# Kernel tuning notes

Hardware: AMD Instinct MI355X
Metric: run time of the kernel (lower is better)

The kernel has to match this reference:

```python
import jax, jax.numpy as jnp
import numpy as np

N_NODES = 50000
N_EDGES = 800000
H = 128            # node_hidden_size
T = 2              # num_prop_rounds


def setup_inputs() -> dict:
    key = jax.random.key(0)
    ks = jax.random.split(key, 10)
    hv = jax.random.normal(ks[0], (N_NODES, H), dtype=jnp.float32)
    he = jax.random.normal(ks[1], (N_EDGES, 1), dtype=jnp.float32)
    src = jax.random.randint(ks[2], (N_EDGES,), 0, N_NODES, dtype=jnp.int32)
    dst = jax.random.randint(ks[3], (N_EDGES,), 0, N_NODES, dtype=jnp.int32)
    # per-round params, stacked on leading T axis; small scale to avoid gate saturation
    W_msg = jax.random.normal(ks[4], (T, 2 * H, 2 * H + 1), dtype=jnp.float32) * 0.05
    b_msg = jax.random.normal(ks[5], (T, 2 * H), dtype=jnp.float32) * 0.05
    W_ih = jax.random.normal(ks[6], (T, 3 * H, 2 * H), dtype=jnp.float32) * 0.05
    W_hh = jax.random.normal(ks[7], (T, 3 * H, H), dtype=jnp.float32) * 0.05
    b_ih = jax.random.normal(ks[8], (T, 3 * H), dtype=jnp.float32) * 0.05
    b_hh = jax.random.normal(ks[9], (T, 3 * H), dtype=jnp.float32) * 0.05
    return dict(hv=hv, he=he, src=src, dst=dst, W_msg=W_msg, b_msg=b_msg,
                W_ih=W_ih, W_hh=W_hh, b_ih=b_ih, b_hh=b_hh)


def _gru_cell(x, h, W_ih, W_hh, b_ih, b_hh):
    # torch.nn.GRUCell math
    gi = x @ W_ih.T + b_ih          # [N, 3H]
    gh = h @ W_hh.T + b_hh          # [N, 3H]
    i_r, i_z, i_n = jnp.split(gi, 3, axis=1)
    h_r, h_z, h_n = jnp.split(gh, 3, axis=1)
    r = jax.nn.sigmoid(i_r + h_r)
    z = jax.nn.sigmoid(i_z + h_z)
    n = jnp.tanh(i_n + r * h_n)
    return (1.0 - z) * n + z * h


def reference(hv, he, src, dst, W_msg, b_msg, W_ih, W_hh, b_ih, b_hh):
    n_nodes = hv.shape[0]
    for t in range(T):
        # per-edge message input: concat([hv_dst, hv_src, he])  [E, 2H+1]
        msg_in = jnp.concatenate([hv[dst], hv[src], he], axis=1)
        edge_act = msg_in @ W_msg[t].T + b_msg[t]          # [E, 2H]
        # ragged sum-reduce over incoming edges (deg-0 nodes get zeros)
        a = jax.ops.segment_sum(edge_act, dst, num_segments=n_nodes)  # [N, 2H]
        hv = _gru_cell(a, hv, W_ih[t], W_hh[t], b_ih[t], b_hh[t])
    return hv
```

## Files before the change

kernel.cpp:

```cpp
#include <hip/hip_runtime.h>
#include <cstdint>
#include <cstddef>

#define N_NODES 50000
#define N_EDGES 800000
#define HDIM 128
#define TROUNDS 2
#define NTILES 3125
#define PACK_PER_T (416 * 64)
#define MAXDEG 64
#define CSTRIDE 16

typedef __attribute__((ext_vector_type(8))) _Float16 half8v;
typedef __attribute__((ext_vector_type(2))) _Float16 half2v;
typedef __attribute__((ext_vector_type(4))) float f32x4;
typedef unsigned short ushort_t;

#define GLD_LDS(gp, lp)                                                        \
  __builtin_amdgcn_global_load_lds(                                            \
      (__attribute__((address_space(1))) const void*)(gp),                     \
      (__attribute__((address_space(3))) void*)(lp), 16, 0, 0)

static __device__ __forceinline__ float sigmoidf_(float x) {
  return 1.0f / (1.0f + __expf(-x));
}
static __device__ __forceinline__ float tanhf_(float x) {
  float xc = fminf(15.0f, fmaxf(-15.0f, x));
  float a = __expf(2.0f * xc);
  return (a - 1.0f) / (a + 1.0f);
}
static __device__ __forceinline__ float f16bits2f(uint32_t hb) {
  ushort_t u = (ushort_t)hb;
  _Float16 h;
  __builtin_memcpy(&h, &u, 2);
  return (float)h;
}

__global__ void pack_all(const float* __restrict__ Wmsg, const float* __restrict__ Wih,
                         const float* __restrict__ Whh, _Float16* __restrict__ W1p,
                         _Float16* __restrict__ W2p, float* __restrict__ we) {
  int g = blockIdx.x * blockDim.x + threadIdx.x;
  if (g < TROUNDS * 256) {
    int t = g >> 8, j = g & 255;
    we[g] = Wmsg[((size_t)t * 256 + j) * 257 + 256];
  }
  if (g >= TROUNDS * PACK_PER_T) return;
  int t = g / PACK_PER_T;
  int r = g % PACK_PER_T;
  int lane = r & 63;
  int fr = r >> 6;
  const float* srcp;
  _Float16* dstp;
  if (fr < 128) {
    int jt = fr >> 3, kt = fr & 7;
    int j = jt * 16 + (lane & 15);
    int k = kt * 32 + ((lane >> 4) << 3);
    srcp = Wmsg + (size_t)t * 256 * 257 + (size_t)j * 257 + k;
    dstp = W1p + ((size_t)t * 128 + fr) * 512 + lane * 8;
  } else {
    int fr2 = fr - 128;
    int chunk = fr2 / 12, idx = fr2 % 12;
    int jt = chunk / 3, pp = chunk % 3;
    int j = pp * 128 + jt * 16 + (lane & 15);
    int k;
    if (idx < 8) {
      k = idx * 32 + ((lane >> 4) << 3);
      srcp = Wih + (size_t)t * 384 * 256 + (size_t)j * 256 + k;
    } else {
      k = (idx - 8) * 32 + ((lane >> 4) << 3);
      srcp = Whh + (size_t)t * 384 * 128 + (size_t)j * 128 + k;
    }
    dstp = W2p + ((size_t)t * 288 + fr2) * 512 + lane * 8;
  }
  #pragma unroll
  for (int e = 0; e < 8; ++e) dstp[e] = (_Float16)srcp[e];
}

__global__ void cast_hv(const float* __restrict__ hv, _Float16* __restrict__ hvh) {
  int i = blockIdx.x * blockDim.x + threadIdx.x;
  if (i >= N_NODES * HDIM / 4) return;
  float4 v = reinterpret_cast<const float4*>(hv)[i];
  half2v o0, o1;
  o0[0] = (_Float16)v.x; o0[1] = (_Float16)v.y;
  o1[0] = (_Float16)v.z; o1[1] = (_Float16)v.w;
  reinterpret_cast<half2v*>(hvh)[i * 2] = o0;
  reinterpret_cast<half2v*>(hvh)[i * 2 + 1] = o1;
}

__global__ void fill_pad(const int* __restrict__ src, const int* __restrict__ dst,
                         const float* __restrict__ he, int* __restrict__ cnt,
                         uint32_t* __restrict__ csr) {
  int e = blockIdx.x * blockDim.x + threadIdx.x;
  if (e >= N_EDGES) return;
  int d = dst[e];
  int slot = atomicAdd(&cnt[(size_t)d * CSTRIDE], 1);
  if (slot < MAXDEG) {
    _Float16 hh = (_Float16)he[e];
    ushort_t hb;
    __builtin_memcpy(&hb, &hh, 2);
    uint32_t en = ((uint32_t)hb << 16) | (uint32_t)src[e];
    csr[(size_t)d * MAXDEG + slot] = en;
  }
}

__global__ void gather_h(const _Float16* __restrict__ hvh, const int* __restrict__ cnt,
                         const uint32_t* __restrict__ csr, _Float16* __restrict__ S_h,
                         float* __restrict__ hsum, float* __restrict__ deg_f, int n) {
  int wid = (int)((blockIdx.x * blockDim.x + threadIdx.x) >> 6);
  int lane = threadIdx.x & 63;
  if (wid >= n) return;
  int deg = min(cnt[(size_t)wid * CSTRIDE], MAXDEG);
  uint32_t ent = (lane < deg) ? csr[(size_t)wid * MAXDEG + lane] : 0u;
  float a0 = 0.f, a1 = 0.f, hs = 0.f;
  int k = 0;
  for (; k + 7 < deg; k += 8) {
    uint32_t ee[8];
    #pragma unroll
    for (int q = 0; q < 8; ++q) ee[q] = __shfl(ent, k + q);
    half2v vv[8];
    #pragma unroll
    for (int q = 0; q < 8; ++q)
      vv[q] = *reinterpret_cast<const half2v*>(hvh + (size_t)(ee[q] & 0xffffu) * HDIM + lane * 2);
    #pragma unroll
    for (int q = 0; q < 8; ++q) {
      a0 += (float)vv[q][0];
      a1 += (float)vv[q][1];
      hs += f16bits2f(ee[q] >> 16);
    }
  }
  for (; k < deg; ++k) {
    uint32_t e0 = __shfl(ent, k);
    half2v v0 = *reinterpret_cast<const half2v*>(hvh + (size_t)(e0 & 0xffffu) * HDIM + lane * 2);
    a0 += (float)v0[0];
    a1 += (float)v0[1];
    hs += f16bits2f(e0 >> 16);
  }
  half2v o;
  o[0] = (_Float16)a0;
  o[1] = (_Float16)a1;
  *reinterpret_cast<half2v*>(S_h + (size_t)wid * HDIM + lane * 2) = o;
  if (lane == 0) hsum[wid] = hs;
  if (lane == 1) deg_f[wid] = (float)deg;
}

__global__ __launch_bounds__(256, 4) void u1_kernel(
    const float* __restrict__ hv, const _Float16* __restrict__ S_h,
    const float* __restrict__ deg_f, const float* __restrict__ hsum,
    const _Float16* __restrict__ W1p, const float* __restrict__ we,
    const float* __restrict__ bmsg, _Float16* __restrict__ a_out) {
  __shared__ _Float16 buf[2][8 * 512];
  const int tid = threadIdx.x;
  const int wv = tid >> 6, lane = tid & 63;
  const int tile = blockIdx.x * 4 + wv;
  const bool act = (tile < NTILES);
  const int rowA = tile * 16 + (lane & 15);
  const int koff = (lane >> 4) * 8;
  const int m0 = (lane >> 4) * 4;

  {
    const _Float16* g = W1p + (size_t)(wv * 2) * 512 + lane * 8;
    #pragma unroll
    for (int i = 0; i < 2; ++i) GLD_LDS(g + i * 512, &buf[0][(wv * 2 + i) * 512]);
  }

  half8v x[8];
  float degs[4], hss[4];
  if (act) {
    float deg = deg_f[rowA];
    const float* hrow = hv + (size_t)rowA * HDIM;
    #pragma unroll
    for (int kt = 0; kt < 4; ++kt) {
      const float* sp = hrow + kt * 32 + koff;
      #pragma unroll
      for (int e = 0; e < 8; ++e) x[kt][e] = (_Float16)(sp[e] * deg);
    }
    const _Float16* srow = S_h + (size_t)rowA * HDIM + koff;
    #pragma unroll
    for (int kt = 0; kt < 4; ++kt)
      x[4 + kt] = *reinterpret_cast<const half8v*>(srow + kt * 32);
    #pragma unroll
    for (int rr = 0; rr < 4; ++rr) {
      degs[rr] = deg_f[tile * 16 + m0 + rr];
      hss[rr] = hsum[tile * 16 + m0 + rr];
    }
  }

  #pragma unroll 1
  for (int jt = 0; jt < 16; ++jt) {
    __syncthreads();
    if (jt < 15) {
      const _Float16* g = W1p + (size_t)(jt + 1) * 4096 + (size_t)(wv * 2) * 512 + lane * 8;
      #pragma unroll
      for (int i = 0; i < 2; ++i) GLD_LDS(g + i * 512, &buf[(jt + 1) & 1][(wv * 2 + i) * 512]);
    }
    const _Float16* B = &buf[jt & 1][0];
    f32x4 acc = {0.f, 0.f, 0.f, 0.f};
    #pragma unroll
    for (int kt = 0; kt < 8; ++kt) {
      half8v b = *reinterpret_cast<const half8v*>(B + (size_t)kt * 512 + lane * 8);
      acc = __builtin_amdgcn_mfma_f32_16x16x32_f16(x[kt], b, acc, 0, 0, 0);
    }
    if (act) {
      int j = jt * 16 + (lane & 15);
      float bm = bmsg[j], w = we[j];
      #pragma unroll
      for (int rr = 0; rr < 4; ++rr)
        a_out[(size_t)(tile * 16 + m0 + rr) * 256 + j] =
            (_Float16)(acc[rr] + degs[rr] * bm + hss[rr] * w);
    }
  }
}

__global__ __launch_bounds__(256, 4) void u2_kernel(
    const float* __restrict__ hv_in, const _Float16* __restrict__ a_in,
    const _Float16* __restrict__ W2p, const float* __restrict__ bih,
    const float* __restrict__ bhh, float* __restrict__ hv_out,
    _Float16* __restrict__ hvh_out) {
  __shared__ _Float16 buf[2][12 * 512];
  const int tid = threadIdx.x;
  const int wv = tid >> 6, lane = tid & 63;
  const int tile = blockIdx.x * 4 + wv;
  const bool act = (tile < NTILES);
  const int rowA = tile * 16 + (lane & 15);
  const int koff = (lane >> 4) * 8;
  const int m0 = (lane >> 4) * 4;

  auto stage = [&](int n) {
    const _Float16* g = W2p + (size_t)n * 6144 + (size_t)(wv * 3) * 512 + lane * 8;
    _Float16* l = &buf[n & 1][(wv * 3) * 512];
    #pragma unroll
    for (int i = 0; i < 3; ++i) GLD_LDS(g + i * 512, l + i * 512);
  };

  stage(0);

  half8v a8[8], h4[4];
  if (act) {
    const _Float16* ar = a_in + (size_t)rowA * 256 + koff;
    #pragma unroll
    for (int kt = 0; kt < 8; ++kt)
      a8[kt] = *reinterpret_cast<const half8v*>(ar + kt * 32);
    const float* hr = hv_in + (size_t)rowA * HDIM + koff;
    #pragma unroll
    for (int kt = 0; kt < 4; ++kt) {
      #pragma unroll
      for (int e = 0; e < 8; ++e) h4[kt][e] = (_Float16)hr[kt * 32 + e];
    }
  }

  auto compute = [&](const _Float16* B, f32x4& ai, f32x4& ag) {
    ai = (f32x4){0.f, 0.f, 0.f, 0.f};
    ag = (f32x4){0.f, 0.f, 0.f, 0.f};
    #pragma unroll
    for (int kt = 0; kt < 8; ++kt) {
      half8v b = *reinterpret_cast<const half8v*>(B + (size_t)kt * 512 + lane * 8);
      ai = __builtin_amdgcn_mfma_f32_16x16x32_f16(a8[kt], b, ai, 0, 0, 0);
    }
    #pragma unroll
    for (int kt = 0; kt < 4; ++kt) {
      half8v b = *reinterpret_cast<const half8v*>(B + (size_t)(8 + kt) * 512 + lane * 8);
      ag = __builtin_amdgcn_mfma_f32_16x16x32_f16(h4[kt], b, ag, 0, 0, 0);
    }
  };

  f32x4 rreg, zreg, ai, ag;
  #pragma unroll 1
  for (int jt = 0; jt < 8; ++jt) {
    const int c0 = jt * 3;
    const int fcol = jt * 16 + (lane & 15);
    __syncthreads();
    stage(c0 + 1);
    compute(&buf[c0 & 1][0], ai, ag);
    if (act) {
      float bi = bih[fcol], bq = bhh[fcol];
      #pragma unroll
      for (int rr = 0; rr < 4; ++rr) rreg[rr] = sigmoidf_(ai[rr] + bi + ag[rr] + bq);
    }
    __syncthreads();
    stage(c0 + 2);
    compute(&buf[(c0 + 1) & 1][0], ai, ag);
    if (act) {
      float bi = bih[128 + fcol], bq = bhh[128 + fcol];
      #pragma unroll
      for (int rr = 0; rr < 4; ++rr) zreg[rr] = sigmoidf_(ai[rr] + bi + ag[rr] + bq);
    }
    __syncthreads();
    if (jt < 7) stage(c0 + 3);
    compute(&buf[(c0 + 2) & 1][0], ai, ag);
    if (act) {
      float bi = bih[256 + fcol], bq = bhh[256 + fcol];
      #pragma unroll
      for (int rr = 0; rr < 4; ++rr) {
        int node = tile * 16 + m0 + rr;
        float n = tanhf_(ai[rr] + bi + rreg[rr] * (ag[rr] + bq));
        float h = hv_in[(size_t)node * HDIM + fcol];
        float hn = (1.f - zreg[rr]) * n + zreg[rr] * h;
        hv_out[(size_t)node * HDIM + fcol] = hn;
        hvh_out[(size_t)node * HDIM + fcol] = (_Float16)hn;
      }
    }
  }
}

extern "C" void kernel_launch(void* const* d_in, const int* in_sizes, int n_in,
                              void* d_out, int out_size, void* d_ws, size_t ws_size,
                              hipStream_t stream) {
  const float* hv   = (const float*)d_in[0];
  const float* he   = (const float*)d_in[1];
  const int*   src  = (const int*)d_in[2];
  const int*   dst  = (const int*)d_in[3];
  const float* Wmsg = (const float*)d_in[4];
  const float* bmsg = (const float*)d_in[5];
  const float* Wih  = (const float*)d_in[6];
  const float* Whh  = (const float*)d_in[7];
  const float* bih  = (const float*)d_in[8];
  const float* bhh  = (const float*)d_in[9];

  char* p = (char*)d_ws;
  auto alloc = [&](size_t bytes) { char* r = p; p += (bytes + 255) & ~(size_t)255; return r; };
  _Float16* S_h   = (_Float16*)alloc((size_t)N_NODES * HDIM * 2);
  _Float16* a_buf = (_Float16*)alloc((size_t)N_NODES * 256 * 2);
  _Float16* hvh   = (_Float16*)alloc((size_t)N_NODES * HDIM * 2);
  float*    deg_f = (float*)alloc((size_t)N_NODES * 4);
  float*    hsum  = (float*)alloc((size_t)N_NODES * 4);
  float*    we    = (float*)alloc((size_t)TROUNDS * 256 * 4);
  const size_t W1PT = (size_t)128 * 512;
  const size_t W2PT = (size_t)288 * 512;
  _Float16* W1p = (_Float16*)alloc(TROUNDS * W1PT * 2);
  _Float16* W2p = (_Float16*)alloc(TROUNDS * W2PT * 2);
  int*      cnt = (int*)alloc((size_t)N_NODES * CSTRIDE * 4);
  uint32_t* csr = (uint32_t*)alloc((size_t)N_NODES * MAXDEG * 4);

  hipMemsetAsync(cnt, 0, (size_t)N_NODES * CSTRIDE * 4, stream);

  pack_all<<<(TROUNDS * PACK_PER_T + 255) / 256, 256, 0, stream>>>(Wmsg, Wih, Whh, W1p, W2p, we);
  cast_hv<<<(N_NODES * HDIM / 4 + 255) / 256, 256, 0, stream>>>(hv, hvh);
  fill_pad<<<(N_EDGES + 255) / 256, 256, 0, stream>>>(src, dst, he, cnt, csr);

  const float* hcur = hv;
  float* outp = (float*)d_out;
  const int ugrid = (NTILES + 3) / 4;
  for (int t = 0; t < TROUNDS; ++t) {
    gather_h<<<(N_NODES + 3) / 4, 256, 0, stream>>>(hvh, cnt, csr, S_h, hsum, deg_f, N_NODES);
    u1_kernel<<<ugrid, 256, 0, stream>>>(
        hcur, S_h, deg_f, hsum, W1p + (size_t)t * W1PT,
        we + (size_t)t * 256, bmsg + (size_t)t * 256, a_buf);
    u2_kernel<<<ugrid, 256, 0, stream>>>(
        hcur, a_buf, W2p + (size_t)t * W2PT,
        bih + (size_t)t * 384, bhh + (size_t)t * 384, outp, hvh);
    hcur = outp;
  }
  (void)in_sizes; (void)n_in; (void)out_size; (void)ws_size;
}
```

Before: 248.4 us.

## Replace global-atomic CSR fill with two-pass bucketed binning by destination

The per-edge global atomic slot assignment into a padded per-node count array is replaced by a two-stage binning scheme. Edges are first grouped per block into 196 buckets of 256 destination nodes using LDS histograms and a prefix scan, then written contiguously into per-bucket global arrays. A second kernel places each bucket's edges into the padded CSR using LDS atomics and writes a compact degree array. The goal is to cut scattered global atomics and the memset of the strided count array, at the cost of an extra pass over an 8-byte-per-edge intermediate buffer and a fixed bucket capacity that could overflow for skewed inputs.

```diff
diff --git a/kernel.cpp b/kernel.cpp
--- a/kernel.cpp
+++ b/kernel.cpp
@@ -9,12 +9,16 @@
 #define NTILES 3125
 #define PACK_PER_T (416 * 64)
 #define MAXDEG 64
-#define CSTRIDE 16
+#define NBUK 196
+#define BCAP 4608
+#define BCE 2048
+#define NBC ((N_EDGES + BCE - 1) / BCE)
 
 typedef __attribute__((ext_vector_type(8))) _Float16 half8v;
 typedef __attribute__((ext_vector_type(2))) _Float16 half2v;
 typedef __attribute__((ext_vector_type(4))) float f32x4;
 typedef unsigned short ushort_t;
+typedef unsigned long long u64;
 
 #define GLD_LDS(gp, lp)                                                        \
   __builtin_amdgcn_global_load_lds(                                            \
@@ -87,29 +91,95 @@
   reinterpret_cast<half2v*>(hvh)[i * 2 + 1] = o1;
 }
 
-__global__ void fill_pad(const int* __restrict__ src, const int* __restrict__ dst,
-                         const float* __restrict__ he, int* __restrict__ cnt,
-                         uint32_t* __restrict__ csr) {
-  int e = blockIdx.x * blockDim.x + threadIdx.x;
-  if (e >= N_EDGES) return;
-  int d = dst[e];
-  int slot = atomicAdd(&cnt[(size_t)d * CSTRIDE], 1);
-  if (slot < MAXDEG) {
-    _Float16 hh = (_Float16)he[e];
-    ushort_t hb;
-    __builtin_memcpy(&hb, &hh, 2);
-    uint32_t en = ((uint32_t)hb << 16) | (uint32_t)src[e];
-    csr[(size_t)d * MAXDEG + slot] = en;
-  }
-}
-
-__global__ void gather_h(const _Float16* __restrict__ hvh, const int* __restrict__ cnt,
+__global__ __launch_bounds__(256) void bin_count(
+    const int* __restrict__ src, const int* __restrict__ dst,
+    const float* __restrict__ he, int* __restrict__ bcur, u64* __restrict__ barr) {
+  __shared__ int hist[256];
+  __shared__ int incl[256];
+  __shared__ int cur[256];
+  __shared__ int gbase[256];
+  __shared__ u64 staged[BCE];
+  const int tid = threadIdx.x;
+  const int e0 = blockIdx.x * BCE;
+  const int tot = min(BCE, N_EDGES - e0);
+
+  hist[tid] = 0;
+  __syncthreads();
+
+  u64 rec[BCE / 256];
+  int nmine = 0;
+  #pragma unroll
+  for (int q = 0; q < BCE / 256; ++q) {
+    int e = e0 + q * 256 + tid;
+    if (e < N_EDGES) {
+      uint32_t d = (uint32_t)dst[e];
+      uint32_t s = (uint32_t)src[e];
+      _Float16 hh = (_Float16)he[e];
+      ushort_t hb;
+      __builtin_memcpy(&hb, &hh, 2);
+      rec[nmine] = ((u64)d << 32) | ((u64)hb << 16) | (u64)s;
+      atomicAdd(&hist[d >> 8], 1);
+      ++nmine;
+    }
+  }
+  __syncthreads();
+
+  incl[tid] = hist[tid];
+  __syncthreads();
+  for (int off = 1; off < 256; off <<= 1) {
+    int v = incl[tid];
+    int a = (tid >= off) ? incl[tid - off] : 0;
+    __syncthreads();
+    incl[tid] = v + a;
+    __syncthreads();
+  }
+  cur[tid] = incl[tid] - hist[tid];
+  __syncthreads();
+
+  for (int q = 0; q < nmine; ++q) {
+    int b = (int)(rec[q] >> 40);
+    int pos = atomicAdd(&cur[b], 1);
+    staged[pos] = rec[q];
+  }
+  if (tid < NBUK && hist[tid] > 0) gbase[tid] = atomicAdd(&bcur[tid], hist[tid]);
+  __syncthreads();
+
+  for (int i = tid; i < tot; i += 256) {
+    u64 r = staged[i];
+    int b = (int)(r >> 40);
+    int excl = incl[b] - hist[b];
+    barr[(size_t)b * BCAP + gbase[b] + (i - excl)] = r;
+  }
+}
+
+__global__ __launch_bounds__(256) void bin_place(
+    const int* __restrict__ bcur, const u64* __restrict__ barr,
+    uint32_t* __restrict__ csr, int* __restrict__ deg_i) {
+  __shared__ int lcnt[256];
+  const int b = blockIdx.x;
+  const int tid = threadIdx.x;
+  const int cnt = bcur[b];
+  lcnt[tid] = 0;
+  __syncthreads();
+  const u64* bp = barr + (size_t)b * BCAP;
+  for (int i = tid; i < cnt; i += 256) {
+    u64 r = bp[i];
+    int d = (int)((r >> 32) & 0xffffu);
+    int slot = atomicAdd(&lcnt[d & 255], 1);
+    if (slot < MAXDEG) csr[(size_t)d * MAXDEG + slot] = (uint32_t)r;
+  }
+  __syncthreads();
+  int node = b * 256 + tid;
+  if (node < N_NODES) deg_i[node] = min(lcnt[tid], MAXDEG);
+}
+
+__global__ void gather_h(const _Float16* __restrict__ hvh, const int* __restrict__ deg_i,
                          const uint32_t* __restrict__ csr, _Float16* __restrict__ S_h,
                          float* __restrict__ hsum, float* __restrict__ deg_f, int n) {
   int wid = (int)((blockIdx.x * blockDim.x + threadIdx.x) >> 6);
   int lane = threadIdx.x & 63;
   if (wid >= n) return;
-  int deg = min(cnt[(size_t)wid * CSTRIDE], MAXDEG);
+  int deg = deg_i[wid];
   uint32_t ent = (lane < deg) ? csr[(size_t)wid * MAXDEG + lane] : 0u;
   float a0 = 0.f, a1 = 0.f, hs = 0.f;
   int k = 0;
@@ -328,20 +398,23 @@
   const size_t W2PT = (size_t)288 * 512;
   _Float16* W1p = (_Float16*)alloc(TROUNDS * W1PT * 2);
   _Float16* W2p = (_Float16*)alloc(TROUNDS * W2PT * 2);
-  int*      cnt = (int*)alloc((size_t)N_NODES * CSTRIDE * 4);
-  uint32_t* csr = (uint32_t*)alloc((size_t)N_NODES * MAXDEG * 4);
-
-  hipMemsetAsync(cnt, 0, (size_t)N_NODES * CSTRIDE * 4, stream);
+  int*      deg_i = (int*)alloc((size_t)N_NODES * 4);
+  int*      bcur  = (int*)alloc((size_t)NBUK * 4);
+  u64*      barr  = (u64*)alloc((size_t)NBUK * BCAP * 8);
+  uint32_t* csr   = (uint32_t*)alloc((size_t)N_NODES * MAXDEG * 4);
+
+  hipMemsetAsync(bcur, 0, (size_t)NBUK * 4, stream);
 
   pack_all<<<(TROUNDS * PACK_PER_T + 255) / 256, 256, 0, stream>>>(Wmsg, Wih, Whh, W1p, W2p, we);
   cast_hv<<<(N_NODES * HDIM / 4 + 255) / 256, 256, 0, stream>>>(hv, hvh);
-  fill_pad<<<(N_EDGES + 255) / 256, 256, 0, stream>>>(src, dst, he, cnt, csr);
+  bin_count<<<NBC, 256, 0, stream>>>(src, dst, he, bcur, barr);
+  bin_place<<<NBUK, 256, 0, stream>>>(bcur, barr, csr, deg_i);
 
   const float* hcur = hv;
   float* outp = (float*)d_out;
   const int ugrid = (NTILES + 3) / 4;
   for (int t = 0; t < TROUNDS; ++t) {
-    gather_h<<<(N_NODES + 3) / 4, 256, 0, stream>>>(hvh, cnt, csr, S_h, hsum, deg_f, N_NODES);
+    gather_h<<<(N_NODES + 3) / 4, 256, 0, stream>>>(hvh, deg_i, csr, S_h, hsum, deg_f, N_NODES);
     u1_kernel<<<ugrid, 256, 0, stream>>>(
         hcur, S_h, deg_f, hsum, W1p + (size_t)t * W1PT,
         we + (size_t)t * 256, bmsg + (size_t)t * 256, a_buf);
```

New measurement: 225.1 us. 1.1x faster.
